# Optimization experiments

Hardware: AMD Instinct MI355X
Metric: run time of the kernel (lower is better)

## Reference

```python
import jax, jax.numpy as jnp
import numpy as np

EPS = 1e-12  # F.normalize eps


def _l2norm(v, axis):
    n = jnp.sqrt(jnp.sum(v * v, axis=axis, keepdims=True))
    return v / jnp.maximum(n, EPS)


def setup_inputs() -> dict:
    key = jax.random.key(0)
    k1, k2, k3, k4 = jax.random.split(key, 4)
    N, C, H, W = 48, 512, 40, 40
    K = 64
    x = jax.random.normal(k1, (N, C, H, W), dtype=jnp.float32)
    conv_w = jax.random.normal(k2, (K, C), dtype=jnp.float32) * 0.02   # cluster-assign 1x1 conv, no bias (vladv2=False)
    attn_w = jax.random.normal(k3, (1, C), dtype=jnp.float32) * 0.02   # heatmap 1x1 conv
    attn_b = jnp.zeros((1,), dtype=jnp.float32)
    centroids = jax.random.uniform(k4, (K, C), dtype=jnp.float32)      # torch.rand init
    return {"x": x, "conv_w": conv_w, "attn_w": attn_w, "attn_b": attn_b, "centroids": centroids}


def reference(x, conv_w, attn_w, attn_b, centroids):
    N, C, H, W = x.shape
    K = conv_w.shape[0]
    P = H * W

    # attention heatmap: ReLU -> 1x1 conv -> ReLU  => [N, 1, H, W]
    hmp = jax.nn.relu(jnp.einsum('nchw,oc->nohw', jax.nn.relu(x), attn_w) + attn_b[None, :, None, None])
    hmp_flat = hmp.reshape(N, 1, P)  # [N,1,P]

    # normalize input descriptors across channels
    xn = _l2norm(x, axis=1)                      # [N,C,H,W]
    x_flat = xn.reshape(N, C, P)                 # [N,C,P]

    # soft assignment: 1x1 conv over clusters + softmax over cluster dim
    logits = jnp.einsum('ncp,kc->nkp', x_flat, conv_w)   # [N,K,P]
    soft_assign = jax.nn.softmax(logits, axis=1)          # softmax over K

    # weighted residual aggregation, fused:
    # vlad[n,k,c] = sum_p (x[n,c,p] - centroids[k,c]) * sa[n,k,p] * hmp[n,0,p]
    w = soft_assign * hmp_flat                            # [N,K,P]
    term1 = jnp.einsum('nkp,ncp->nkc', w, x_flat)         # [N,K,C]
    wsum = jnp.sum(w, axis=-1)                            # [N,K]
    vlad = term1 - wsum[:, :, None] * centroids[None, :, :]

    vlad = _l2norm(vlad, axis=2)                          # intra-normalize per cluster
    vlad = vlad.reshape(N, K * C)
    vlad = _l2norm(vlad, axis=1)                          # global L2 normalize
    return vlad
```

## Files before the change

kernel.cpp:

```cpp
#include <hip/hip_runtime.h>
#include <math.h>

#define NN 48
#define CC 512
#define KK 64
#define PP 1600
#define EPSF 1e-12f

typedef short short8 __attribute__((ext_vector_type(8)));
typedef float f32x4 __attribute__((ext_vector_type(4)));

static __device__ __forceinline__ unsigned short f2bf(float f) {
    unsigned u = __float_as_uint(f);
    u += 0x7fffu + ((u >> 16) & 1u);
    return (unsigned short)(u >> 16);
}
static __device__ __forceinline__ unsigned pack2(float a, float b) {
    return (unsigned)f2bf(a) | ((unsigned)f2bf(b) << 16);
}

__global__ __launch_bounds__(256, 4) void kn_logits(
    const float* __restrict__ x, const float* __restrict__ conv_w,
    const float* __restrict__ attn_w, const float* __restrict__ attn_b,
    unsigned short* __restrict__ wg, float* __restrict__ wsum,
    unsigned short* __restrict__ xbf)
{
    __shared__ unsigned short xt[64][76];
    __shared__ unsigned short cwb[64][72];
    __shared__ float attn_l[CC];
    __shared__ float red[16][64];
    __shared__ float invn_l[64];
    __shared__ float hmp_l[64];
    __shared__ float wsum_l[KK];

    const int n = blockIdx.y, p0 = blockIdx.x * 64, tid = threadIdx.x;
    const int q = tid & 15, cg = tid >> 4;
    const int wave = tid >> 6, lane = tid & 63;
    const int lq = lane >> 4, lm = lane & 15;
    const int kr = tid >> 2, cq = tid & 3;

    for (int i = tid; i < CC; i += 256) attn_l[i] = attn_w[i];
    if (tid < KK) wsum_l[tid] = 0.f;

    f32x4 acc[4];
#pragma unroll
    for (int mt = 0; mt < 4; ++mt) acc[mt] = (f32x4){0.f, 0.f, 0.f, 0.f};
    float ss[4] = {0.f, 0.f, 0.f, 0.f};
    float ad[4] = {0.f, 0.f, 0.f, 0.f};

    const float* xb = x + (size_t)n * CC * PP;
    const float* wp0 = conv_w + (size_t)kr * CC + cq * 16;
    const float* xp0 = xb + (size_t)(cg * 4) * PP + p0 + 4 * q;

    float4 wv[4], xv[4];
#pragma unroll
    for (int j = 0; j < 4; ++j) wv[j] = *(const float4*)(wp0 + 4 * j);
#pragma unroll
    for (int j = 0; j < 4; ++j) xv[j] = *(const float4*)(xp0 + (size_t)j * PP);

    __syncthreads();

#pragma unroll 1
    for (int cs = 0; cs < 8; ++cs) {
        float4 wn[4], xn_[4];
        if (cs < 7) {
            const float* wp = wp0 + (cs + 1) * 64;
            const float* xp = xp0 + (size_t)(cs + 1) * 64 * PP;
#pragma unroll
            for (int j = 0; j < 4; ++j) wn[j] = *(const float4*)(wp + 4 * j);
#pragma unroll
            for (int j = 0; j < 4; ++j) xn_[j] = *(const float4*)(xp + (size_t)j * PP);
        }
#pragma unroll
        for (int j = 0; j < 4; ++j) {
            uint2 u = {pack2(wv[j].x, wv[j].y), pack2(wv[j].z, wv[j].w)};
            *(uint2*)&cwb[kr][cq * 16 + 4 * j] = u;
        }
        const int cbase = cs * 64 + cg * 4;
#pragma unroll
        for (int j = 0; j < 4; ++j) {
            float4 v = xv[j];
            const float aw = attn_l[cbase + j];
            ss[0] += v.x * v.x; ss[1] += v.y * v.y;
            ss[2] += v.z * v.z; ss[3] += v.w * v.w;
            ad[0] += fmaxf(v.x, 0.f) * aw; ad[1] += fmaxf(v.y, 0.f) * aw;
            ad[2] += fmaxf(v.z, 0.f) * aw; ad[3] += fmaxf(v.w, 0.f) * aw;
            uint2 u = {pack2(v.x, v.y), pack2(v.z, v.w)};
            *(uint2*)&xt[cg * 4 + j][4 * q] = u;
            if (xbf)
                *(uint2*)(xbf + ((size_t)n * CC + cbase + j) * PP + p0 + 4 * q) = u;
        }
        __syncthreads();
#pragma unroll
        for (int ks = 0; ks < 2; ++ks) {
            short8 af[4];
#pragma unroll
            for (int mt = 0; mt < 4; ++mt)
                af[mt] = *(const short8*)&cwb[mt * 16 + lm][ks * 32 + lq * 8];
            const int pl = wave * 16 + lm;
            const int cb = ks * 32 + lq * 8;
            short8 bv;
#pragma unroll
            for (int j = 0; j < 8; ++j) bv[j] = (short)xt[cb + j][pl];
#pragma unroll
            for (int mt = 0; mt < 4; ++mt)
                acc[mt] = __builtin_amdgcn_mfma_f32_16x16x32_bf16(
                    af[mt], bv, acc[mt], 0, 0, 0);
        }
        __syncthreads();
        if (cs < 7) {
#pragma unroll
            for (int j = 0; j < 4; ++j) { wv[j] = wn[j]; xv[j] = xn_[j]; }
        }
    }

#pragma unroll
    for (int j = 0; j < 4; ++j) red[cg][4 * q + j] = ss[j];
    __syncthreads();
    if (tid < 64) {
        float S = 0.f;
#pragma unroll
        for (int l = 0; l < 16; ++l) S += red[l][tid];
        invn_l[tid] = 1.f / fmaxf(sqrtf(S), EPSF);
    }
    __syncthreads();
#pragma unroll
    for (int j = 0; j < 4; ++j) red[cg][4 * q + j] = ad[j];
    __syncthreads();
    if (tid < 64) {
        float A = 0.f;
#pragma unroll
        for (int l = 0; l < 16; ++l) A += red[l][tid];
        hmp_l[tid] = fmaxf(A + attn_b[0], 0.f);
    }
    __syncthreads();

    const int pl = wave * 16 + lm;
    const float inv = invn_l[pl];
    const float hp = hmp_l[pl];
    float mx = -1e30f;
#pragma unroll
    for (int mt = 0; mt < 4; ++mt)
#pragma unroll
        for (int r = 0; r < 4; ++r) {
            const float l = acc[mt][r] * inv;
            acc[mt][r] = l;
            mx = fmaxf(mx, l);
        }
    mx = fmaxf(mx, __shfl_xor(mx, 16));
    mx = fmaxf(mx, __shfl_xor(mx, 32));
    float s = 0.f;
#pragma unroll
    for (int mt = 0; mt < 4; ++mt)
#pragma unroll
        for (int r = 0; r < 4; ++r) {
            const float e = __expf(acc[mt][r] - mx);
            acc[mt][r] = e;
            s += e;
        }
    s += __shfl_xor(s, 16);
    s += __shfl_xor(s, 32);
    const float sden = hp / s;

    unsigned short* wrb = wg + (size_t)n * KK * PP + p0;
#pragma unroll
    for (int mt = 0; mt < 4; ++mt)
#pragma unroll
        for (int r = 0; r < 4; ++r) {
            const int k = mt * 16 + lq * 4 + r;
            const float w0 = acc[mt][r] * sden;
            float wk = w0;
#pragma unroll
            for (int o = 1; o < 16; o <<= 1) wk += __shfl_xor(wk, o);
            if (lm == 0) atomicAdd(&wsum_l[k], wk);
            wrb[(size_t)k * PP + pl] = f2bf(w0 * inv);
        }
    __syncthreads();
    if (tid < KK) atomicAdd(&wsum[n * KK + tid], wsum_l[tid]);
}

template <bool XB>
__global__ __launch_bounds__(256) void kn_term1(
    const float* __restrict__ xf, const unsigned short* __restrict__ xbf,
    const unsigned short* __restrict__ wgq, float* __restrict__ term1p)
{
    __shared__ unsigned short wt[64][40];
    __shared__ unsigned short xt2[64][40];
    const int c0 = blockIdx.x * 64, n = blockIdx.y, ph = blockIdx.z;
    const int tid = threadIdx.x;
    const int wave = tid >> 6, lane = tid & 63, lq = lane >> 4, lm = lane & 15;
    const int koff = (wave >> 1) * 32, coff = (wave & 1) * 32;
    const int s_begin = (50 * ph) >> 2, s_end = (50 * (ph + 1)) >> 2;
    const int rA = tid >> 2, cq = tid & 3;

    f32x4 acc[2][2];
#pragma unroll
    for (int mt = 0; mt < 2; ++mt)
#pragma unroll
        for (int nt = 0; nt < 2; ++nt) acc[mt][nt] = (f32x4){0.f, 0.f, 0.f, 0.f};

    const unsigned short* wb = wgq + (size_t)n * KK * PP + (size_t)rA * PP + cq * 8;
    const unsigned short* xbb = xbf + ((size_t)n * CC + c0 + rA) * PP + cq * 8;
    const float* xfb = xf + ((size_t)n * CC + c0 + rA) * PP + cq * 8;

    auto ldB = [&](int p) -> uint4 {
        if (XB) {
            return *(const uint4*)(xbb + p);
        } else {
            const float* sp = xfb + p;
            float4 a = *(const float4*)sp, b = *(const float4*)(sp + 4);
            return make_uint4(pack2(a.x, a.y), pack2(a.z, a.w),
                              pack2(b.x, b.y), pack2(b.z, b.w));
        }
    };

    uint4 pa = *(const uint4*)(wb + s_begin * 32);
    uint4 pb = ldB(s_begin * 32);

    for (int ps = s_begin; ps < s_end; ++ps) {
        *(uint4*)&wt[rA][cq * 8] = pa;
        *(uint4*)&xt2[rA][cq * 8] = pb;
        __syncthreads();
        if (ps + 1 < s_end) {
            pa = *(const uint4*)(wb + (ps + 1) * 32);
            pb = ldB((ps + 1) * 32);
        }
        short8 af[2], bv[2];
#pragma unroll
        for (int mt = 0; mt < 2; ++mt)
            af[mt] = *(const short8*)&wt[koff + mt * 16 + lm][lq * 8];
#pragma unroll
        for (int nt = 0; nt < 2; ++nt)
            bv[nt] = *(const short8*)&xt2[coff + nt * 16 + lm][lq * 8];
#pragma unroll
        for (int mt = 0; mt < 2; ++mt)
#pragma unroll
            for (int nt = 0; nt < 2; ++nt)
                acc[mt][nt] = __builtin_amdgcn_mfma_f32_16x16x32_bf16(
                    af[mt], bv[nt], acc[mt][nt], 0, 0, 0);
        __syncthreads();
    }

    float* ob = term1p + ((size_t)ph * NN + n) * KK * CC + c0 + coff;
#pragma unroll
    for (int mt = 0; mt < 2; ++mt)
#pragma unroll
        for (int r = 0; r < 4; ++r) {
            const int k = koff + mt * 16 + lq * 4 + r;
#pragma unroll
            for (int nt = 0; nt < 2; ++nt)
                ob[(size_t)k * CC + nt * 16 + lm] = acc[mt][nt][r];
        }
}

__global__ __launch_bounds__(128) void kn_vlad(
    const float* __restrict__ term1p, const float* __restrict__ wsum,
    const float* __restrict__ cent, float* __restrict__ out,
    float* __restrict__ nsum)
{
    const int k = blockIdx.x, n = blockIdx.y, tid = threadIdx.x;
    const size_t base = ((size_t)n * KK + k) * CC;
    const size_t NKC = (size_t)NN * KK * CC;
    const float ws = wsum[n * KK + k];
    const int c = tid * 4;

    float4 ce = *(const float4*)(cent + (size_t)k * CC + c);
    float4 v = {-ws * ce.x, -ws * ce.y, -ws * ce.z, -ws * ce.w};
#pragma unroll
    for (int h = 0; h < 4; ++h) {
        float4 a = *(const float4*)(term1p + h * NKC + base + c);
        v.x += a.x; v.y += a.y; v.z += a.z; v.w += a.w;
    }

    float s = v.x * v.x + v.y * v.y + v.z * v.z + v.w * v.w;
#pragma unroll
    for (int o = 32; o >= 1; o >>= 1) s += __shfl_down(s, o, 64);

    __shared__ float rb[2];
    __shared__ float sinv;
    if ((tid & 63) == 0) rb[tid >> 6] = s;
    __syncthreads();
    if (tid == 0) {
        const float S = rb[0] + rb[1];
        const float inv = 1.f / fmaxf(sqrtf(S), EPSF);
        sinv = inv;
        atomicAdd(&nsum[n], S * inv * inv);
    }
    __syncthreads();
    const float inv = sinv;
    float4 o4 = {v.x * inv, v.y * inv, v.z * inv, v.w * inv};
    *(float4*)(out + base + c) = o4;
}

__global__ __launch_bounds__(256) void kn_scale(
    float* __restrict__ out, const float* __restrict__ nsum)
{
    const int n = blockIdx.y;
    const size_t off = ((size_t)blockIdx.x * 256 + threadIdx.x) * 4;
    const float g = 1.f / fmaxf(sqrtf(nsum[n]), EPSF);
    float4 v = *(float4*)(out + (size_t)n * KK * CC + off);
    v.x *= g; v.y *= g; v.z *= g; v.w *= g;
    *(float4*)(out + (size_t)n * KK * CC + off) = v;
}

extern "C" void kernel_launch(void* const* d_in, const int* in_sizes, int n_in,
                              void* d_out, int out_size, void* d_ws, size_t ws_size,
                              hipStream_t stream)
{
    (void)in_sizes; (void)n_in; (void)out_size;
    const float* x      = (const float*)d_in[0];
    const float* conv_w = (const float*)d_in[1];
    const float* attn_w = (const float*)d_in[2];
    const float* attn_b = (const float*)d_in[3];
    const float* cent   = (const float*)d_in[4];
    float* out = (float*)d_out;

    char* w = (char*)d_ws;
    float* term1p = (float*)w;            w += (size_t)4 * NN * KK * CC * 4;
    float* wsum   = (float*)w;            w += (size_t)NN * KK * 4;
    float* nsum   = (float*)w;            w += 256;
    unsigned short* wg  = (unsigned short*)w; w += (size_t)NN * KK * PP * 2;
    unsigned short* xbf = (unsigned short*)w;
    const size_t need_xb = (size_t)(w - (char*)d_ws) + (size_t)NN * CC * PP * 2;
    const bool xb = ws_size >= need_xb;

    hipMemsetAsync(wsum, 0, NN * KK * sizeof(float), stream);
    hipMemsetAsync(nsum, 0, NN * sizeof(float), stream);

    kn_logits<<<dim3(25, NN), 256, 0, stream>>>(x, conv_w, attn_w, attn_b,
                                                wg, wsum, xb ? xbf : nullptr);
    if (xb)
        kn_term1<true><<<dim3(8, NN, 4), 256, 0, stream>>>(x, xbf, wg, term1p);
    else
        kn_term1<false><<<dim3(8, NN, 4), 256, 0, stream>>>(x, xbf, wg, term1p);
    kn_vlad <<<dim3(KK, NN), 128, 0, stream>>>(term1p, wsum, cent, out, nsum);
    kn_scale<<<dim3(32, NN), 256, 0, stream>>>(out, nsum);
}
```

Before: 322.2 us.

## Drop bf16 x copy, prefetch earlier in term1, fold global norm into constant

kn_logits no longer writes a bf16 copy of x. kn_term1 now always reads fp32 x and converts it to bf16 on the fly, trading the extra write and read of that copy for a larger fp32 read. The next tile's global loads in kn_term1 are issued before the LDS stores and barrier, to hide more load latency. The global L2 normalization is replaced by a constant factor of 1/8, since 64 intra-normalized cluster rows have a total norm of 8. This removes the kn_scale kernel, the nsum atomics and a memset. The constant is only exact when no cluster row has a near-zero norm.

```diff
diff --git a/kernel.cpp b/kernel.cpp
--- a/kernel.cpp
+++ b/kernel.cpp
@@ -22,8 +22,7 @@
 __global__ __launch_bounds__(256, 4) void kn_logits(
     const float* __restrict__ x, const float* __restrict__ conv_w,
     const float* __restrict__ attn_w, const float* __restrict__ attn_b,
-    unsigned short* __restrict__ wg, float* __restrict__ wsum,
-    unsigned short* __restrict__ xbf)
+    unsigned short* __restrict__ wg, float* __restrict__ wsum)
 {
     __shared__ unsigned short xt[64][76];
     __shared__ unsigned short cwb[64][72];
@@ -87,8 +86,6 @@
             ad[2] += fmaxf(v.z, 0.f) * aw; ad[3] += fmaxf(v.w, 0.f) * aw;
             uint2 u = {pack2(v.x, v.y), pack2(v.z, v.w)};
             *(uint2*)&xt[cg * 4 + j][4 * q] = u;
-            if (xbf)
-                *(uint2*)(xbf + ((size_t)n * CC + cbase + j) * PP + p0 + 4 * q) = u;
         }
         __syncthreads();
 #pragma unroll
@@ -179,10 +176,9 @@
     if (tid < KK) atomicAdd(&wsum[n * KK + tid], wsum_l[tid]);
 }
 
-template <bool XB>
 __global__ __launch_bounds__(256) void kn_term1(
-    const float* __restrict__ xf, const unsigned short* __restrict__ xbf,
-    const unsigned short* __restrict__ wgq, float* __restrict__ term1p)
+    const float* __restrict__ xf, const unsigned short* __restrict__ wgq,
+    float* __restrict__ term1p)
 {
     __shared__ unsigned short wt[64][40];
     __shared__ unsigned short xt2[64][40];
@@ -200,31 +196,27 @@
         for (int nt = 0; nt < 2; ++nt) acc[mt][nt] = (f32x4){0.f, 0.f, 0.f, 0.f};
 
     const unsigned short* wb = wgq + (size_t)n * KK * PP + (size_t)rA * PP + cq * 8;
-    const unsigned short* xbb = xbf + ((size_t)n * CC + c0 + rA) * PP + cq * 8;
     const float* xfb = xf + ((size_t)n * CC + c0 + rA) * PP + cq * 8;
 
     auto ldB = [&](int p) -> uint4 {
-        if (XB) {
-            return *(const uint4*)(xbb + p);
-        } else {
-            const float* sp = xfb + p;
-            float4 a = *(const float4*)sp, b = *(const float4*)(sp + 4);
-            return make_uint4(pack2(a.x, a.y), pack2(a.z, a.w),
-                              pack2(b.x, b.y), pack2(b.z, b.w));
-        }
+        const float* sp = xfb + p;
+        float4 a = *(const float4*)sp, b = *(const float4*)(sp + 4);
+        return make_uint4(pack2(a.x, a.y), pack2(a.z, a.w),
+                          pack2(b.x, b.y), pack2(b.z, b.w));
     };
 
     uint4 pa = *(const uint4*)(wb + s_begin * 32);
     uint4 pb = ldB(s_begin * 32);
 
     for (int ps = s_begin; ps < s_end; ++ps) {
+        uint4 na, nb;
+        if (ps + 1 < s_end) {
+            na = *(const uint4*)(wb + (ps + 1) * 32);
+            nb = ldB((ps + 1) * 32);
+        }
         *(uint4*)&wt[rA][cq * 8] = pa;
         *(uint4*)&xt2[rA][cq * 8] = pb;
         __syncthreads();
-        if (ps + 1 < s_end) {
-            pa = *(const uint4*)(wb + (ps + 1) * 32);
-            pb = ldB((ps + 1) * 32);
-        }
         short8 af[2], bv[2];
 #pragma unroll
         for (int mt = 0; mt < 2; ++mt)
@@ -239,6 +231,7 @@
                 acc[mt][nt] = __builtin_amdgcn_mfma_f32_16x16x32_bf16(
                     af[mt], bv[nt], acc[mt][nt], 0, 0, 0);
         __syncthreads();
+        pa = na; pb = nb;
     }
 
     float* ob = term1p + ((size_t)ph * NN + n) * KK * CC + c0 + coff;
@@ -255,8 +248,7 @@
 
 __global__ __launch_bounds__(128) void kn_vlad(
     const float* __restrict__ term1p, const float* __restrict__ wsum,
-    const float* __restrict__ cent, float* __restrict__ out,
-    float* __restrict__ nsum)
+    const float* __restrict__ cent, float* __restrict__ out)
 {
     const int k = blockIdx.x, n = blockIdx.y, tid = threadIdx.x;
     const size_t base = ((size_t)n * KK + k) * CC;
@@ -282,32 +274,19 @@
     __syncthreads();
     if (tid == 0) {
         const float S = rb[0] + rb[1];
-        const float inv = 1.f / fmaxf(sqrtf(S), EPSF);
-        sinv = inv;
-        atomicAdd(&nsum[n], S * inv * inv);
+        sinv = 0.125f / fmaxf(sqrtf(S), EPSF);
     }
     __syncthreads();
     const float inv = sinv;
     float4 o4 = {v.x * inv, v.y * inv, v.z * inv, v.w * inv};
     *(float4*)(out + base + c) = o4;
-}
-
-__global__ __launch_bounds__(256) void kn_scale(
-    float* __restrict__ out, const float* __restrict__ nsum)
-{
-    const int n = blockIdx.y;
-    const size_t off = ((size_t)blockIdx.x * 256 + threadIdx.x) * 4;
-    const float g = 1.f / fmaxf(sqrtf(nsum[n]), EPSF);
-    float4 v = *(float4*)(out + (size_t)n * KK * CC + off);
-    v.x *= g; v.y *= g; v.z *= g; v.w *= g;
-    *(float4*)(out + (size_t)n * KK * CC + off) = v;
 }
 
 extern "C" void kernel_launch(void* const* d_in, const int* in_sizes, int n_in,
                               void* d_out, int out_size, void* d_ws, size_t ws_size,
                               hipStream_t stream)
 {
-    (void)in_sizes; (void)n_in; (void)out_size;
+    (void)in_sizes; (void)n_in; (void)out_size; (void)ws_size;
     const float* x      = (const float*)d_in[0];
     const float* conv_w = (const float*)d_in[1];
     const float* attn_w = (const float*)d_in[2];
@@ -318,21 +297,12 @@
     char* w = (char*)d_ws;
     float* term1p = (float*)w;            w += (size_t)4 * NN * KK * CC * 4;
     float* wsum   = (float*)w;            w += (size_t)NN * KK * 4;
-    float* nsum   = (float*)w;            w += 256;
-    unsigned short* wg  = (unsigned short*)w; w += (size_t)NN * KK * PP * 2;
-    unsigned short* xbf = (unsigned short*)w;
-    const size_t need_xb = (size_t)(w - (char*)d_ws) + (size_t)NN * CC * PP * 2;
-    const bool xb = ws_size >= need_xb;
+    unsigned short* wg = (unsigned short*)w;
 
     hipMemsetAsync(wsum, 0, NN * KK * sizeof(float), stream);
-    hipMemsetAsync(nsum, 0, NN * sizeof(float), stream);
 
     kn_logits<<<dim3(25, NN), 256, 0, stream>>>(x, conv_w, attn_w, attn_b,
-                                                wg, wsum, xb ? xbf : nullptr);
-    if (xb)
-        kn_term1<true><<<dim3(8, NN, 4), 256, 0, stream>>>(x, xbf, wg, term1p);
-    else
-        kn_term1<false><<<dim3(8, NN, 4), 256, 0, stream>>>(x, xbf, wg, term1p);
-    kn_vlad <<<dim3(KK, NN), 128, 0, stream>>>(term1p, wsum, cent, out, nsum);
-    kn_scale<<<dim3(32, NN), 256, 0, stream>>>(out, nsum);
-}
+                                                wg, wsum);
+    kn_term1<<<dim3(8, NN, 4), 256, 0, stream>>>(x, wg, term1p);
+    kn_vlad <<<dim3(KK, NN), 128, 0, stream>>>(term1p, wsum, cent, out);
+}
```

Result: faster. 300.8 us (-6.6%).
